# Performance work log

Hardware: AMD Instinct MI355X
Metric: run time of the kernel (lower is better)

Reference implementation:

```python
import jax, jax.numpy as jnp
import numpy as np

# Coefficient form of the 16 differentiable binary logic ops:
# op(a,b) = c0 + c1*a + c2*b + c3*a*b  (algebraically identical to bin_op_s's stacked einsum)
_COEF_NP = np.array([
    [0, 0, 0, 0],    # 0: zeros
    [0, 0, 0, 1],    # 1: a*b
    [0, 1, 0, -1],   # 2: a*(1-b)
    [0, 1, 0, 0],    # 3: a
    [0, 0, 1, -1],   # 4: (1-a)*b
    [0, 0, 1, 0],    # 5: b
    [0, 1, 1, -2],   # 6: xor
    [0, 1, 1, -1],   # 7: or
    [1, -1, -1, 1],  # 8: nor
    [1, -1, -1, 2],  # 9: xnor
    [1, 0, -1, 0],   # 10: 1-b
    [1, 0, -1, 1],   # 11: b=>a
    [1, -1, 0, 0],   # 12: 1-a
    [1, -1, 0, 1],   # 13: a=>b
    [1, 0, 0, -1],   # 14: nand
    [1, 0, 0, 0],    # 15: ones
], dtype=np.float32)
COEF = jnp.asarray(_COEF_NP)

TREE_DEPTH = 3
NUM_CLASSES = 10
TAU = 10.0
K = 32
BATCH = 128


def _conv_tree(x, leaf_idx, w):
    # x: [B,C,H,W]; leaf_idx: [O,8] int32 into C*9 unfolded patch dim; w: [O,7,16]
    B, C, H, W = x.shape
    xp = jnp.pad(x, ((0, 0), (0, 0), (1, 1), (1, 1)))
    # unfold (kernel=3, stride=1, pad=1): torch ordering is c*9 + spatial
    pats = jnp.stack([xp[:, :, di:di + H, dj:dj + W]
                      for di in range(3) for dj in range(3)], axis=2)  # [B,C,9,H,W]
    pats = pats.reshape(B, C * 9, H * W).transpose(0, 2, 1)            # [B,L,C*9]
    cur = pats[:, :, leaf_idx]                                         # [B,L,O,8]
    sw = jax.nn.softmax(w, axis=-1)                                    # training-mode soft gates
    coef = jnp.einsum('ogk,kc->ogc', sw, COEF)                         # [O,7,4]
    for level in range(TREE_DEPTH):
        a = cur[..., 0::2]
        b = cur[..., 1::2]                                             # [B,L,O,n]
        n = a.shape[-1]
        off = 2 ** level - 1                                           # faithful to original gate indexing
        c = coef[:, off:off + n]                                       # [O,n,4]
        cur = c[..., 0] + c[..., 1] * a + c[..., 2] * b + c[..., 3] * (a * b)
    out = cur[..., 0]                                                  # [B,L,O]
    return out.transpose(0, 2, 1).reshape(B, -1, H, W)


def _orpool(x):
    B, C, H, W = x.shape
    return x.reshape(B, C, H // 2, 2, W // 2, 2).max(axis=(3, 5))


def _difflogic(x, ca, cb, w):
    # x: [B,D]; ca/cb: [O]; w: [O,16]
    a = x[:, ca]
    b = x[:, cb]
    c = jax.nn.softmax(w, axis=-1) @ COEF                              # [O,4]
    return c[:, 0] + c[:, 1] * a + c[:, 2] * b + c[:, 3] * (a * b)


def _forward(x, w1, w2, w3, w4, fw1, fw2, fw3,
             l1, l2, l3, l4, ca1, cb1, ca2, cb2, ca3, cb3):
    # threshold-encode to 9 binary channels (bilinear resize to 32x32 is identity here)
    xb = jnp.concatenate([(x > (i + 1) / 4).astype(jnp.float32) for i in range(3)], axis=1)
    h = xb
    for li, w in ((l1, w1), (l2, w2), (l3, w3), (l4, w4)):
        h = _orpool(_conv_tree(h, li, w))
    h = h.reshape(h.shape[0], -1)                                      # [B, 4096]
    h = _difflogic(h, ca1, cb1, fw1)
    h = _difflogic(h, ca2, cb2, fw2)
    h = _difflogic(h, ca3, cb3, fw3)
    return h.reshape(h.shape[0], NUM_CLASSES, -1).sum(-1) / TAU


def _make_leaf_idx(in_ch, out_ch, rng):
    idx = np.zeros((out_ch, 8), np.int32)
    for c in range(out_ch):
        chans = rng.permutation(in_ch)[:2]
        parts = [ch * 9 + rng.permutation(9)[:4] for ch in chans]
        idx[c] = np.concatenate(parts)
    return jnp.asarray(idx)


def _unique_connections(in_dim, out_dim, rng):
    x = np.arange(in_dim, dtype=np.int64)
    a, b = x[::2], x[1::2]
    m = min(len(a), len(b)); a, b = a[:m], b[:m]
    if len(a) < out_dim:
        a = np.concatenate([a, x[1::2]]); b = np.concatenate([b, x[2::2]])
        m = min(len(a), len(b)); a, b = a[:m], b[:m]
    offset = 2
    while out_dim > len(a) > offset:
        a = np.concatenate([a, x[:-offset]]); b = np.concatenate([b, x[offset:]])
        offset += 1
    a, b = a[:out_dim], b[:out_dim]
    perm = rng.permutation(out_dim)
    return jnp.asarray(a[perm]), jnp.asarray(b[perm])


def setup_inputs() -> dict:
    key = jax.random.key(0)
    rng = np.random.default_rng(0)
    ks = jax.random.split(key, 8)
    x = jax.random.uniform(ks[0], (BATCH, 3, 32, 32), dtype=jnp.float32)
    chans = [(9, K), (K, 4 * K), (4 * K, 16 * K), (16 * K, 32 * K)]
    w1, w2, w3, w4 = [jax.random.normal(ks[1 + i], (oc, 7, 16), dtype=jnp.float32)
                      for i, (_, oc) in enumerate(chans)]
    l1, l2, l3, l4 = [_make_leaf_idx(ic, oc, rng) for ic, oc in chans]
    fc_in = 32 * K * 4
    fdims = [(fc_in, 1280 * K), (1280 * K, 640 * K), (640 * K, 320 * K)]
    fw1, fw2, fw3 = [jax.random.normal(ks[5 + i], (od, 16), dtype=jnp.float32)
                     for i, (_, od) in enumerate(fdims)]
    (ca1, cb1), (ca2, cb2), (ca3, cb3) = [_unique_connections(i, o, rng) for i, o in fdims]
    return dict(x=x, w1=w1, w2=w2, w3=w3, w4=w4, fw1=fw1, fw2=fw2, fw3=fw3,
                l1=l1, l2=l2, l3=l3, l4=l4,
                ca1=ca1, cb1=cb1, ca2=ca2, cb2=cb2, ca3=ca3, cb3=cb3)


def reference(x, w1, w2, w3, w4, fw1, fw2, fw3,
              l1, l2, l3, l4, ca1, cb1, ca2, cb2, ca3, cb3):
    return _forward(x, w1, w2, w3, w4, fw1, fw2, fw3,
                    l1, l2, l3, l4, ca1, cb1, ca2, cb2, ca3, cb3)
```

## Files before the change

kernel.cpp:

```cpp
#include <hip/hip_runtime.h>
#include <math.h>


typedef _Float16 h2 __attribute__((ext_vector_type(2)));

__constant__ float c_coef_tbl[16][4] = {
    {0, 0, 0, 0}, {0, 0, 0, 1}, {0, 1, 0, -1}, {0, 1, 0, 0},
    {0, 0, 1, -1}, {0, 0, 1, 0}, {0, 1, 1, -2}, {0, 1, 1, -1},
    {1, -1, -1, 1}, {1, -1, -1, 2}, {1, 0, -1, 0}, {1, 0, -1, 1},
    {1, -1, 0, 0}, {1, -1, 0, 1}, {1, 0, 0, -1}, {1, 0, 0, 0}};

__device__ __forceinline__ float4 softmax_coef(const float* __restrict__ wr) {
  float m = -1e30f;
#pragma unroll
  for (int k = 0; k < 16; ++k) m = fmaxf(m, wr[k]);
  float e[16], s = 0.f;
#pragma unroll
  for (int k = 0; k < 16; ++k) { e[k] = __expf(wr[k] - m); s += e[k]; }
  float inv = 1.f / s;
  float c0 = 0.f, c1 = 0.f, c2 = 0.f, c3 = 0.f;
#pragma unroll
  for (int k = 0; k < 16; ++k) {
    c0 += e[k] * c_coef_tbl[k][0];
    c1 += e[k] * c_coef_tbl[k][1];
    c2 += e[k] * c_coef_tbl[k][2];
    c3 += e[k] * c_coef_tbl[k][3];
  }
  return make_float4(c0 * inv, c1 * inv, c2 * inv, c3 * inv);
}

__device__ __forceinline__ float gate_eval(float4 c, float a, float b) {
  return c.x + c.y * a + c.z * b + c.w * (a * b);
}

__global__ void prep_all(const float* __restrict__ w1, const float* __restrict__ w2,
                         const float* __restrict__ w3, const float* __restrict__ w4,
                         const float* __restrict__ fw1, const float* __restrict__ fw2,
                         const float* __restrict__ fw3,
                         const int* __restrict__ ca1, const int* __restrict__ cb1,
                         const int* __restrict__ ca2, const int* __restrict__ cb2,
                         const int* __restrict__ ca3, const int* __restrict__ cb3,
                         float4* __restrict__ coefC,
                         unsigned short* __restrict__ midx16,
                         _Float16* __restrict__ mcoefh) {
  int g = blockIdx.x * blockDim.x + threadIdx.x;
  if (g < 71680) {
    int o = g / 7;
    int s = g - o * 7;
    float4 c;
    if (s < 4) {
      int k = (s < 2) ? ca3[o] : cb3[o];
      int j = (s & 1) ? cb2[k] : ca2[k];
      midx16[o * 8 + s * 2]     = (unsigned short)ca1[j];
      midx16[o * 8 + s * 2 + 1] = (unsigned short)cb1[j];
      c = softmax_coef(fw1 + j * 16);
    } else if (s < 6) {
      int k = (s == 4) ? ca3[o] : cb3[o];
      c = softmax_coef(fw2 + k * 16);
    } else {
      c = softmax_coef(fw3 + o * 16);
    }
    _Float16* mc = mcoefh + o * 28 + s * 4;
    mc[0] = (_Float16)c.x; mc[1] = (_Float16)c.y;
    mc[2] = (_Float16)c.z; mc[3] = (_Float16)c.w;
  } else if (g < 78464) {
    int gg = g - 71680;
    int base = gg;
    const float* w;
    if (gg < 128)       {               w = w1; }
    else if (gg < 640)  { gg -= 128;    w = w2; }
    else if (gg < 2688) { gg -= 640;    w = w3; }
    else                { gg -= 2688;   w = w4; }
    coefC[base] = softmax_coef(w + ((gg >> 2) * 7 + (gg & 3)) * 16);
  }
}

__device__ __forceinline__ h2 gateh(const h2* c, h2 a, h2 b) {
  return c[0] + c[1] * a + c[2] * b + c[3] * (a * b);
}

__device__ __forceinline__ float4 dec_cf(uint2 u) {
  h2 p0, p1;
  *(unsigned*)&p0 = u.x;
  *(unsigned*)&p1 = u.y;
  return make_float4((float)p0[0], (float)p0[1], (float)p1[0], (float)p1[1]);
}

template <int C, int H, int W, int OC, bool DUP>
__device__ void stage(const h2* __restrict__ in, h2* __restrict__ outD,
                      _Float16* __restrict__ outP,
                      const int* __restrict__ leaf,
                      const float4* __restrict__ coef, int tid) {
  constexpr int Hp = H + 2, Wp = W + 2;
  constexpr int PH = H / 2, PW = W / 2;
  constexpr int NPOS = PH * PW;
  constexpr int TPO = 1024 / OC;
  constexpr int ITER = NPOS / TPO;
  constexpr int OWp = PW + 2;
  constexpr int OHWp = (PH + 2) * (PW + 2);

  int oc = tid / TPO;
  int lane = tid % TPO;

  int toff[8];
#pragma unroll
  for (int l = 0; l < 8; ++l) {
    int k = leaf[oc * 8 + l];
    int cc = k / 9;
    int p = k - 9 * cc;
    int di = p / 3;
    int dj = p - 3 * di;
    toff[l] = cc * (Hp * Wp) + di * Wp + dj;
  }
  h2 ch[4][4];
#pragma unroll
  for (int r = 0; r < 4; ++r) {
    float4 c = coef[oc * 4 + r];
    _Float16 x0 = (_Float16)c.x, x1 = (_Float16)c.y,
             x2 = (_Float16)c.z, x3 = (_Float16)c.w;
    ch[r][0][0] = x0; ch[r][0][1] = x0;
    ch[r][1][0] = x1; ch[r][1][1] = x1;
    ch[r][2][0] = x2; ch[r][2][1] = x2;
    ch[r][3][0] = x3; ch[r][3][1] = x3;
  }

#pragma unroll
  for (int it = 0; it < ITER; ++it) {
    int pos = lane + it * TPO;
    int pw = pos % PW, ph = pos / PW;
    h2 o01[2];
#pragma unroll
    for (int py = 0; py < 2; ++py) {
      int pbase = (2 * ph + py) * Wp + 2 * pw;
      h2 lv[8];
#pragma unroll
      for (int l = 0; l < 8; ++l) lv[l] = in[toff[l] + pbase];
      h2 t0 = gateh(ch[0], lv[0], lv[1]);
      h2 t1 = gateh(ch[1], lv[2], lv[3]);
      h2 t2 = gateh(ch[2], lv[4], lv[5]);
      h2 t3 = gateh(ch[3], lv[6], lv[7]);
      h2 u0 = gateh(ch[1], t0, t1);
      h2 u1 = gateh(ch[2], t2, t3);
      o01[py] = gateh(ch[3], u0, u1);
    }
    _Float16 m0 = o01[0][0] > o01[1][0] ? o01[0][0] : o01[1][0];
    _Float16 m1 = o01[0][1] > o01[1][1] ? o01[0][1] : o01[1][1];
    _Float16 v = m0 > m1 ? m0 : m1;
    if (DUP) {
      _Float16* oh = (_Float16*)outD;
      int cell = oc * OHWp + (ph + 1) * OWp + (pw + 1);
      oh[2 * cell] = v;
      oh[2 * cell - 1] = v;
    } else {
      outP[oc * NPOS + ph * PW + pw] = v;
    }
  }
}

__device__ __forceinline__ void zero_h2(h2* p, int n, int tid) {
  for (int i = tid; i < n; i += 1024) p[i] = h2{(_Float16)0, (_Float16)0};
}

__global__ __launch_bounds__(1024) void mega(
    const float* __restrict__ x, const float4* __restrict__ coefC,
    const int* __restrict__ l1, const int* __restrict__ l2,
    const int* __restrict__ l3, const int* __restrict__ l4,
    const unsigned short* __restrict__ midx16,
    const _Float16* __restrict__ mcoefh, float* __restrict__ out) {
  __shared__ h2 A[12800];
  __shared__ h2 B[18432];
  __shared__ float red[16][10];
  int tid = threadIdx.x;
  int b = blockIdx.x;

  zero_h2(A, 10404, tid);
  zero_h2(B, 10368, tid);
  __syncthreads();
  const float* xb_ = x + b * 3072;
  for (int cell = tid; cell < 9 * 34 * 34; cell += 1024) {
    int j = cell % 34;
    int t = cell / 34;
    int i = t % 34;
    int c9 = t / 34;
    int th = c9 / 3, c = c9 - 3 * th;
    float thr = (float)(th + 1) * 0.25f;
    _Float16 lo = (_Float16)0, hi = (_Float16)0;
    if (i >= 1 && i <= 32) {
      const float* row = xb_ + c * 1024 + (i - 1) * 32;
      if (j >= 1 && j <= 32) lo = (_Float16)((row[j - 1] > thr) ? 1.f : 0.f);
      if (j <= 31)           hi = (_Float16)((row[j] > thr) ? 1.f : 0.f);
    }
    A[cell] = h2{lo, hi};
  }
  __syncthreads();

  stage<9, 32, 32, 32, true>(A, B, nullptr, l1, coefC, tid);
  __syncthreads();
  zero_h2(A, 12800, tid);
  __syncthreads();
  stage<32, 16, 16, 128, true>(B, A, nullptr, l2, coefC + 128, tid);
  __syncthreads();
  zero_h2(B, 18432, tid);
  __syncthreads();
  stage<128, 8, 8, 512, true>(A, B, nullptr, l3, coefC + 640, tid);
  __syncthreads();
  _Float16* Ah = (_Float16*)A;
  stage<512, 4, 4, 1024, false>(B, nullptr, Ah, l4, coefC + 2688, tid);
  __syncthreads();

  const uint4* mi = (const uint4*)midx16;
  const uint2* mc = (const uint2*)mcoefh;
  int wid = tid >> 6;
#pragma unroll
  for (int k = 0; k < 10; ++k) {
    int o = k * 1024 + tid;
    uint4 I = mi[o];
    const uint2* cfp = mc + o * 7;
    float L0 = gate_eval(dec_cf(cfp[0]), (float)Ah[I.x & 0xffff], (float)Ah[I.x >> 16]);
    float L1 = gate_eval(dec_cf(cfp[1]), (float)Ah[I.y & 0xffff], (float)Ah[I.y >> 16]);
    float L2 = gate_eval(dec_cf(cfp[2]), (float)Ah[I.z & 0xffff], (float)Ah[I.z >> 16]);
    float L3 = gate_eval(dec_cf(cfp[3]), (float)Ah[I.w & 0xffff], (float)Ah[I.w >> 16]);
    float M0 = gate_eval(dec_cf(cfp[4]), L0, L1);
    float M1 = gate_eval(dec_cf(cfp[5]), L2, L3);
    float y = gate_eval(dec_cf(cfp[6]), M0, M1);
#pragma unroll
    for (int m = 32; m > 0; m >>= 1) y += __shfl_xor(y, m, 64);
    if ((tid & 63) == 0) red[wid][k] = y;
  }
  __syncthreads();
  if (tid < 10) {
    float s = 0.f;
#pragma unroll
    for (int w = 0; w < 16; ++w) s += red[w][tid];
    out[b * 10 + tid] = s * 0.1f;
  }
}

extern "C" void kernel_launch(void* const* d_in, const int* in_sizes, int n_in,
                              void* d_out, int out_size, void* d_ws, size_t ws_size,
                              hipStream_t stream) {
  const float* x   = (const float*)d_in[0];
  const float* w1  = (const float*)d_in[1];
  const float* w2  = (const float*)d_in[2];
  const float* w3  = (const float*)d_in[3];
  const float* w4  = (const float*)d_in[4];
  const float* fw1 = (const float*)d_in[5];
  const float* fw2 = (const float*)d_in[6];
  const float* fw3 = (const float*)d_in[7];
  const int* l1  = (const int*)d_in[8];
  const int* l2  = (const int*)d_in[9];
  const int* l3  = (const int*)d_in[10];
  const int* l4  = (const int*)d_in[11];
  const int* ca1 = (const int*)d_in[12];
  const int* cb1 = (const int*)d_in[13];
  const int* ca2 = (const int*)d_in[14];
  const int* cb2 = (const int*)d_in[15];
  const int* ca3 = (const int*)d_in[16];
  const int* cb3 = (const int*)d_in[17];

  char* ws = (char*)d_ws;
  float4*         coefC  = (float4*)ws;
  unsigned short* midx16 = (unsigned short*)(ws + 108544);
  _Float16*       mcoefh = (_Float16*)(ws + 108544 + 163840);

  prep_all<<<307, 256, 0, stream>>>(w1, w2, w3, w4, fw1, fw2, fw3,
                                    ca1, cb1, ca2, cb2, ca3, cb3,
                                    coefC, midx16, mcoefh);
  mega<<<128, 1024, 0, stream>>>(x, coefC, l1, l2, l3, l4, midx16, mcoefh,
                                 (float*)d_out);
}
```

Measured before the change: 62.84 us.

## Split each sample across two cooperative blocks with global-memory stages and pair flags

Replaces the one-block-per-sample LDS megakernel with a cooperative launch of 256 blocks, where two blocks share each sample and each computes half the output channels of every conv stage. Intermediate activations move from shared memory to global workspace, and a pairwise flag barrier synchronises the partner blocks between stages. The conv stages also switch from packed half2 math on padded layouts to scalar fp32 gate evaluation with explicit bounds checks, and binarisation is fused into stage 1. This is meant to use all CUs, but it adds global-memory traffic, spin-wait synchronisation and recomputation of leaf offsets per job.

```diff
diff --git a/kernel.cpp b/kernel.cpp
--- a/kernel.cpp
+++ b/kernel.cpp
@@ -2,7 +2,10 @@
 #include <math.h>
 
 
-typedef _Float16 h2 __attribute__((ext_vector_type(2)));
+typedef _Float16 h16;
+typedef _Float16 h2v __attribute__((ext_vector_type(2)));
+
+#define NTHR 1024
 
 __constant__ float c_coef_tbl[16][4] = {
     {0, 0, 0, 0}, {0, 0, 0, 1}, {0, 1, 0, -1}, {0, 1, 0, 0},
@@ -31,6 +34,12 @@
 
 __device__ __forceinline__ float gate_eval(float4 c, float a, float b) {
   return c.x + c.y * a + c.z * b + c.w * (a * b);
+}
+__device__ __forceinline__ float4 dec_cf(uint2 u) {
+  h2v p0, p1;
+  *(unsigned*)&p0 = u.x;
+  *(unsigned*)&p1 = u.y;
+  return make_float4((float)p0[0], (float)p0[1], (float)p1[0], (float)p1[1]);
 }
 
 __global__ void prep_all(const float* __restrict__ w1, const float* __restrict__ w2,
@@ -42,8 +51,10 @@
                          const int* __restrict__ ca3, const int* __restrict__ cb3,
                          float4* __restrict__ coefC,
                          unsigned short* __restrict__ midx16,
-                         _Float16* __restrict__ mcoefh) {
+                         _Float16* __restrict__ mcoefh,
+                         unsigned int* __restrict__ flags) {
   int g = blockIdx.x * blockDim.x + threadIdx.x;
+  if (g < 256) flags[g] = 0u;
   if (g < 71680) {
     int o = g / 7;
     int s = g - o * 7;
@@ -67,172 +78,150 @@
     int gg = g - 71680;
     int base = gg;
     const float* w;
-    if (gg < 128)       {               w = w1; }
-    else if (gg < 640)  { gg -= 128;    w = w2; }
-    else if (gg < 2688) { gg -= 640;    w = w3; }
-    else                { gg -= 2688;   w = w4; }
+    if (gg < 128)       {             w = w1; }
+    else if (gg < 640)  { gg -= 128;  w = w2; }
+    else if (gg < 2688) { gg -= 640;  w = w3; }
+    else                { gg -= 2688; w = w4; }
     coefC[base] = softmax_coef(w + ((gg >> 2) * 7 + (gg & 3)) * 16);
   }
 }
 
-__device__ __forceinline__ h2 gateh(const h2* c, h2 a, h2 b) {
-  return c[0] + c[1] * a + c[2] * b + c[3] * (a * b);
-}
-
-__device__ __forceinline__ float4 dec_cf(uint2 u) {
-  h2 p0, p1;
-  *(unsigned*)&p0 = u.x;
-  *(unsigned*)&p1 = u.y;
-  return make_float4((float)p0[0], (float)p0[1], (float)p1[0], (float)p1[1]);
-}
-
-template <int C, int H, int W, int OC, bool DUP>
-__device__ void stage(const h2* __restrict__ in, h2* __restrict__ outD,
-                      _Float16* __restrict__ outP,
-                      const int* __restrict__ leaf,
-                      const float4* __restrict__ coef, int tid) {
-  constexpr int Hp = H + 2, Wp = W + 2;
-  constexpr int PH = H / 2, PW = W / 2;
+__device__ __forceinline__ void psync(unsigned int* flags, int me, int pa,
+                                      unsigned int s, int tid) {
+  __syncthreads();
+  if (tid == 0) {
+    __threadfence();
+    __hip_atomic_store(&flags[me], s, __ATOMIC_RELEASE, __HIP_MEMORY_SCOPE_AGENT);
+    while (__hip_atomic_load(&flags[pa], __ATOMIC_ACQUIRE,
+                             __HIP_MEMORY_SCOPE_AGENT) < s) {
+      __builtin_amdgcn_s_sleep(2);
+    }
+  }
+  __syncthreads();
+}
+
+template <int C, int H, int W, int OC, bool BIN>
+__device__ void stage(const h16* __restrict__ in, const float* __restrict__ xsrc,
+                      h16* __restrict__ outp, const int* __restrict__ leaf,
+                      const float4* __restrict__ coef, int role, int tid) {
+  constexpr int PH = H / 2, PW = W / 2, HW = H * W;
   constexpr int NPOS = PH * PW;
-  constexpr int TPO = 1024 / OC;
-  constexpr int ITER = NPOS / TPO;
-  constexpr int OWp = PW + 2;
-  constexpr int OHWp = (PH + 2) * (PW + 2);
-
-  int oc = tid / TPO;
-  int lane = tid % TPO;
-
-  int toff[8];
-#pragma unroll
-  for (int l = 0; l < 8; ++l) {
-    int k = leaf[oc * 8 + l];
-    int cc = k / 9;
-    int p = k - 9 * cc;
-    int di = p / 3;
-    int dj = p - 3 * di;
-    toff[l] = cc * (Hp * Wp) + di * Wp + dj;
-  }
-  h2 ch[4][4];
-#pragma unroll
-  for (int r = 0; r < 4; ++r) {
-    float4 c = coef[oc * 4 + r];
-    _Float16 x0 = (_Float16)c.x, x1 = (_Float16)c.y,
-             x2 = (_Float16)c.z, x3 = (_Float16)c.w;
-    ch[r][0][0] = x0; ch[r][0][1] = x0;
-    ch[r][1][0] = x1; ch[r][1][1] = x1;
-    ch[r][2][0] = x2; ch[r][2][1] = x2;
-    ch[r][3][0] = x3; ch[r][3][1] = x3;
-  }
-
-#pragma unroll
+  constexpr int NJ = (OC / 2) * NPOS;
+  constexpr int ITER = NJ / NTHR;
+  int ocBase = role * (OC / 2);
+#pragma unroll 2
   for (int it = 0; it < ITER; ++it) {
-    int pos = lane + it * TPO;
+    int job = it * NTHR + tid;
+    int pos = job % NPOS;
+    int oc = ocBase + job / NPOS;
     int pw = pos % PW, ph = pos / PW;
-    h2 o01[2];
+
+    int cc[8], di[8], dj[8];
+#pragma unroll
+    for (int l = 0; l < 8; ++l) {
+      int k = leaf[oc * 8 + l];
+      cc[l] = k / 9;
+      int p = k - 9 * cc[l];
+      di[l] = p / 3;
+      dj[l] = p - 3 * di[l];
+    }
+    float4 c0 = coef[oc * 4 + 0];
+    float4 c1 = coef[oc * 4 + 1];
+    float4 c2 = coef[oc * 4 + 2];
+    float4 c3 = coef[oc * 4 + 3];
+
+    float best = -1e30f;
 #pragma unroll
     for (int py = 0; py < 2; ++py) {
-      int pbase = (2 * ph + py) * Wp + 2 * pw;
-      h2 lv[8];
-#pragma unroll
-      for (int l = 0; l < 8; ++l) lv[l] = in[toff[l] + pbase];
-      h2 t0 = gateh(ch[0], lv[0], lv[1]);
-      h2 t1 = gateh(ch[1], lv[2], lv[3]);
-      h2 t2 = gateh(ch[2], lv[4], lv[5]);
-      h2 t3 = gateh(ch[3], lv[6], lv[7]);
-      h2 u0 = gateh(ch[1], t0, t1);
-      h2 u1 = gateh(ch[2], t2, t3);
-      o01[py] = gateh(ch[3], u0, u1);
-    }
-    _Float16 m0 = o01[0][0] > o01[1][0] ? o01[0][0] : o01[1][0];
-    _Float16 m1 = o01[0][1] > o01[1][1] ? o01[0][1] : o01[1][1];
-    _Float16 v = m0 > m1 ? m0 : m1;
-    if (DUP) {
-      _Float16* oh = (_Float16*)outD;
-      int cell = oc * OHWp + (ph + 1) * OWp + (pw + 1);
-      oh[2 * cell] = v;
-      oh[2 * cell - 1] = v;
-    } else {
-      outP[oc * NPOS + ph * PW + pw] = v;
-    }
-  }
-}
-
-__device__ __forceinline__ void zero_h2(h2* p, int n, int tid) {
-  for (int i = tid; i < n; i += 1024) p[i] = h2{(_Float16)0, (_Float16)0};
-}
-
-__global__ __launch_bounds__(1024) void mega(
+#pragma unroll
+      for (int px = 0; px < 2; ++px) {
+        int i = 2 * ph + py, j = 2 * pw + px;
+        float lv[8];
+#pragma unroll
+        for (int l = 0; l < 8; ++l) {
+          int ii = i + di[l] - 1, jj = j + dj[l] - 1;
+          float v = 0.f;
+          if ((unsigned)ii < (unsigned)H && (unsigned)jj < (unsigned)W) {
+            if (BIN) {
+              int bc = cc[l] % 3;
+              float thr = (float)(cc[l] / 3 + 1) * 0.25f;
+              v = (xsrc[bc * 1024 + ii * 32 + jj] > thr) ? 1.f : 0.f;
+            } else {
+              v = (float)in[cc[l] * HW + ii * W + jj];
+            }
+          }
+          lv[l] = v;
+        }
+        float t0 = gate_eval(c0, lv[0], lv[1]);
+        float t1 = gate_eval(c1, lv[2], lv[3]);
+        float t2 = gate_eval(c2, lv[4], lv[5]);
+        float t3 = gate_eval(c3, lv[6], lv[7]);
+        float u0 = gate_eval(c1, t0, t1);
+        float u1 = gate_eval(c2, t2, t3);
+        best = fmaxf(best, gate_eval(c3, u0, u1));
+      }
+    }
+    outp[oc * NPOS + pos] = (h16)best;
+  }
+}
+
+__global__ __launch_bounds__(1024) void coop(
     const float* __restrict__ x, const float4* __restrict__ coefC,
     const int* __restrict__ l1, const int* __restrict__ l2,
     const int* __restrict__ l3, const int* __restrict__ l4,
     const unsigned short* __restrict__ midx16,
-    const _Float16* __restrict__ mcoefh, float* __restrict__ out) {
-  __shared__ h2 A[12800];
-  __shared__ h2 B[18432];
-  __shared__ float red[16][10];
+    const _Float16* __restrict__ mcoefh,
+    h16* __restrict__ s1, h16* __restrict__ s2,
+    h16* __restrict__ s3, h16* __restrict__ s4,
+    unsigned int* __restrict__ flags, float* __restrict__ out) {
+  __shared__ float red[16];
   int tid = threadIdx.x;
-  int b = blockIdx.x;
-
-  zero_h2(A, 10404, tid);
-  zero_h2(B, 10368, tid);
-  __syncthreads();
-  const float* xb_ = x + b * 3072;
-  for (int cell = tid; cell < 9 * 34 * 34; cell += 1024) {
-    int j = cell % 34;
-    int t = cell / 34;
-    int i = t % 34;
-    int c9 = t / 34;
-    int th = c9 / 3, c = c9 - 3 * th;
-    float thr = (float)(th + 1) * 0.25f;
-    _Float16 lo = (_Float16)0, hi = (_Float16)0;
-    if (i >= 1 && i <= 32) {
-      const float* row = xb_ + c * 1024 + (i - 1) * 32;
-      if (j >= 1 && j <= 32) lo = (_Float16)((row[j - 1] > thr) ? 1.f : 0.f);
-      if (j <= 31)           hi = (_Float16)((row[j] > thr) ? 1.f : 0.f);
-    }
-    A[cell] = h2{lo, hi};
-  }
-  __syncthreads();
-
-  stage<9, 32, 32, 32, true>(A, B, nullptr, l1, coefC, tid);
-  __syncthreads();
-  zero_h2(A, 12800, tid);
-  __syncthreads();
-  stage<32, 16, 16, 128, true>(B, A, nullptr, l2, coefC + 128, tid);
-  __syncthreads();
-  zero_h2(B, 18432, tid);
-  __syncthreads();
-  stage<128, 8, 8, 512, true>(A, B, nullptr, l3, coefC + 640, tid);
-  __syncthreads();
-  _Float16* Ah = (_Float16*)A;
-  stage<512, 4, 4, 1024, false>(B, nullptr, Ah, l4, coefC + 2688, tid);
-  __syncthreads();
+  int me = blockIdx.x;
+  int g = me & 127;
+  int role = me >> 7;
+  int pa = me ^ 128;
+
+  const float* xg = x + g * 3072;
+  h16* b1 = s1 + g * 8192;
+  h16* b2 = s2 + g * 8192;
+  h16* b3 = s3 + g * 8192;
+  h16* b4 = s4 + g * 4096;
+
+  stage<9, 32, 32, 32, true>(nullptr, xg, b1, l1, coefC, role, tid);
+  psync(flags, me, pa, 1, tid);
+  stage<32, 16, 16, 128, false>(b1, nullptr, b2, l2, coefC + 128, role, tid);
+  psync(flags, me, pa, 2, tid);
+  stage<128, 8, 8, 512, false>(b2, nullptr, b3, l3, coefC + 640, role, tid);
+  psync(flags, me, pa, 3, tid);
+  stage<512, 4, 4, 1024, false>(b3, nullptr, b4, l4, coefC + 2688, role, tid);
+  psync(flags, me, pa, 4, tid);
 
   const uint4* mi = (const uint4*)midx16;
   const uint2* mc = (const uint2*)mcoefh;
-  int wid = tid >> 6;
-#pragma unroll
-  for (int k = 0; k < 10; ++k) {
-    int o = k * 1024 + tid;
+#pragma unroll
+  for (int k = 0; k < 5; ++k) {
+    int cls = role * 5 + k;
+    int o = cls * 1024 + tid;
     uint4 I = mi[o];
     const uint2* cfp = mc + o * 7;
-    float L0 = gate_eval(dec_cf(cfp[0]), (float)Ah[I.x & 0xffff], (float)Ah[I.x >> 16]);
-    float L1 = gate_eval(dec_cf(cfp[1]), (float)Ah[I.y & 0xffff], (float)Ah[I.y >> 16]);
-    float L2 = gate_eval(dec_cf(cfp[2]), (float)Ah[I.z & 0xffff], (float)Ah[I.z >> 16]);
-    float L3 = gate_eval(dec_cf(cfp[3]), (float)Ah[I.w & 0xffff], (float)Ah[I.w >> 16]);
+    float L0 = gate_eval(dec_cf(cfp[0]), (float)b4[I.x & 0xffff], (float)b4[I.x >> 16]);
+    float L1 = gate_eval(dec_cf(cfp[1]), (float)b4[I.y & 0xffff], (float)b4[I.y >> 16]);
+    float L2 = gate_eval(dec_cf(cfp[2]), (float)b4[I.z & 0xffff], (float)b4[I.z >> 16]);
+    float L3 = gate_eval(dec_cf(cfp[3]), (float)b4[I.w & 0xffff], (float)b4[I.w >> 16]);
     float M0 = gate_eval(dec_cf(cfp[4]), L0, L1);
     float M1 = gate_eval(dec_cf(cfp[5]), L2, L3);
     float y = gate_eval(dec_cf(cfp[6]), M0, M1);
 #pragma unroll
     for (int m = 32; m > 0; m >>= 1) y += __shfl_xor(y, m, 64);
-    if ((tid & 63) == 0) red[wid][k] = y;
-  }
-  __syncthreads();
-  if (tid < 10) {
-    float s = 0.f;
-#pragma unroll
-    for (int w = 0; w < 16; ++w) s += red[w][tid];
-    out[b * 10 + tid] = s * 0.1f;
+    if ((tid & 63) == 0) red[tid >> 6] = y;
+    __syncthreads();
+    if (tid == 0) {
+      float s = 0.f;
+#pragma unroll
+      for (int w = 0; w < 16; ++w) s += red[w];
+      out[g * 10 + cls] = s * 0.1f;
+    }
+    __syncthreads();
   }
 }
 
@@ -257,15 +246,23 @@
   const int* cb2 = (const int*)d_in[15];
   const int* ca3 = (const int*)d_in[16];
   const int* cb3 = (const int*)d_in[17];
+  float* out = (float*)d_out;
 
   char* ws = (char*)d_ws;
   float4*         coefC  = (float4*)ws;
   unsigned short* midx16 = (unsigned short*)(ws + 108544);
-  _Float16*       mcoefh = (_Float16*)(ws + 108544 + 163840);
+  _Float16*       mcoefh = (_Float16*)(ws + 272384);
+  unsigned int*   flags  = (unsigned int*)(ws + 845824);
+  h16*            s1b    = (h16*)(ws + 846848);
+  h16*            s2b    = (h16*)(ws + 846848 + 2097152);
+  h16*            s3b    = (h16*)(ws + 846848 + 2 * 2097152);
+  h16*            s4b    = (h16*)(ws + 846848 + 3 * 2097152);
 
   prep_all<<<307, 256, 0, stream>>>(w1, w2, w3, w4, fw1, fw2, fw3,
                                     ca1, cb1, ca2, cb2, ca3, cb3,
-                                    coefC, midx16, mcoefh);
-  mega<<<128, 1024, 0, stream>>>(x, coefC, l1, l2, l3, l4, midx16, mcoefh,
-                                 (float*)d_out);
-}
+                                    coefC, midx16, mcoefh, flags);
+
+  void* args[] = {&x, &coefC, &l1, &l2, &l3, &l4, &midx16, &mcoefh,
+                  &s1b, &s2b, &s3b, &s4b, &flags, &out};
+  hipLaunchCooperativeKernel((void*)coop, dim3(256), dim3(1024), args, 0, stream);
+}
```

Result: slower. 161.3 us (+156.7%).

## Split each sample across two cooperative blocks with global-memory staging and pair flags

Applied to the files above, without the earlier changes.

Each batch sample was handled by one 1024-thread block using shared-memory ping-pong buffers. Now two blocks per sample each take half the output channels and half the classes of every stage, doubling the grid to 256 blocks so more CUs are used. Intermediates move from LDS to global workspace, and the paired blocks synchronize through release/acquire flags in a cooperative launch. This trades higher latency on the gather-heavy stage reads, plus the cross-block spin barriers, for twice the parallelism.

```diff
diff --git a/kernel.cpp b/kernel.cpp
--- a/kernel.cpp
+++ b/kernel.cpp
@@ -2,6 +2,7 @@
 #include <math.h>
 
 
+typedef _Float16 h16;
 typedef _Float16 h2 __attribute__((ext_vector_type(2)));
 
 __constant__ float c_coef_tbl[16][4] = {
@@ -31,6 +32,15 @@
 
 __device__ __forceinline__ float gate_eval(float4 c, float a, float b) {
   return c.x + c.y * a + c.z * b + c.w * (a * b);
+}
+__device__ __forceinline__ float4 dec_cf(uint2 u) {
+  h2 p0, p1;
+  *(unsigned*)&p0 = u.x;
+  *(unsigned*)&p1 = u.y;
+  return make_float4((float)p0[0], (float)p0[1], (float)p1[0], (float)p1[1]);
+}
+__device__ __forceinline__ h2 gateh(const h2* c, h2 a, h2 b) {
+  return c[0] + c[1] * a + c[2] * b + c[3] * (a * b);
 }
 
 __global__ void prep_all(const float* __restrict__ w1, const float* __restrict__ w2,
@@ -42,8 +52,10 @@
                          const int* __restrict__ ca3, const int* __restrict__ cb3,
                          float4* __restrict__ coefC,
                          unsigned short* __restrict__ midx16,
-                         _Float16* __restrict__ mcoefh) {
+                         _Float16* __restrict__ mcoefh,
+                         unsigned int* __restrict__ flags) {
   int g = blockIdx.x * blockDim.x + threadIdx.x;
+  if (g < 256) flags[g] = 0u;
   if (g < 71680) {
     int o = g / 7;
     int s = g - o * 7;
@@ -67,39 +79,42 @@
     int gg = g - 71680;
     int base = gg;
     const float* w;
-    if (gg < 128)       {               w = w1; }
-    else if (gg < 640)  { gg -= 128;    w = w2; }
-    else if (gg < 2688) { gg -= 640;    w = w3; }
-    else                { gg -= 2688;   w = w4; }
+    if (gg < 128)       {             w = w1; }
+    else if (gg < 640)  { gg -= 128;  w = w2; }
+    else if (gg < 2688) { gg -= 640;  w = w3; }
+    else                { gg -= 2688; w = w4; }
     coefC[base] = softmax_coef(w + ((gg >> 2) * 7 + (gg & 3)) * 16);
   }
 }
 
-__device__ __forceinline__ h2 gateh(const h2* c, h2 a, h2 b) {
-  return c[0] + c[1] * a + c[2] * b + c[3] * (a * b);
-}
-
-__device__ __forceinline__ float4 dec_cf(uint2 u) {
-  h2 p0, p1;
-  *(unsigned*)&p0 = u.x;
-  *(unsigned*)&p1 = u.y;
-  return make_float4((float)p0[0], (float)p0[1], (float)p1[0], (float)p1[1]);
+__device__ __forceinline__ void psync(unsigned int* flags, int me, int pa,
+                                      unsigned int s, int tid) {
+  __syncthreads();
+  if (tid == 0) {
+    __threadfence();
+    __hip_atomic_store(&flags[me], s, __ATOMIC_RELEASE, __HIP_MEMORY_SCOPE_AGENT);
+    while (__hip_atomic_load(&flags[pa], __ATOMIC_ACQUIRE,
+                             __HIP_MEMORY_SCOPE_AGENT) < s) {
+      __builtin_amdgcn_s_sleep(2);
+    }
+  }
+  __syncthreads();
 }
 
 template <int C, int H, int W, int OC, bool DUP>
 __device__ void stage(const h2* __restrict__ in, h2* __restrict__ outD,
-                      _Float16* __restrict__ outP,
+                      h16* __restrict__ outP,
                       const int* __restrict__ leaf,
-                      const float4* __restrict__ coef, int tid) {
+                      const float4* __restrict__ coef, int role, int tid) {
   constexpr int Hp = H + 2, Wp = W + 2;
   constexpr int PH = H / 2, PW = W / 2;
   constexpr int NPOS = PH * PW;
-  constexpr int TPO = 1024 / OC;
+  constexpr int TPO = 2048 / OC;
   constexpr int ITER = NPOS / TPO;
   constexpr int OWp = PW + 2;
   constexpr int OHWp = (PH + 2) * (PW + 2);
 
-  int oc = tid / TPO;
+  int oc = role * (OC / 2) + tid / TPO;
   int lane = tid % TPO;
 
   int toff[8];
@@ -147,7 +162,7 @@
     _Float16 m1 = o01[0][1] > o01[1][1] ? o01[0][1] : o01[1][1];
     _Float16 v = m0 > m1 ? m0 : m1;
     if (DUP) {
-      _Float16* oh = (_Float16*)outD;
+      h16* oh = (h16*)outD;
       int cell = oc * OHWp + (ph + 1) * OWp + (pw + 1);
       oh[2 * cell] = v;
       oh[2 * cell - 1] = v;
@@ -157,27 +172,39 @@
   }
 }
 
-__device__ __forceinline__ void zero_h2(h2* p, int n, int tid) {
-  for (int i = tid; i < n; i += 1024) p[i] = h2{(_Float16)0, (_Float16)0};
-}
-
-__global__ __launch_bounds__(1024) void mega(
+__global__ __launch_bounds__(1024) void coop(
     const float* __restrict__ x, const float4* __restrict__ coefC,
     const int* __restrict__ l1, const int* __restrict__ l2,
     const int* __restrict__ l3, const int* __restrict__ l4,
     const unsigned short* __restrict__ midx16,
-    const _Float16* __restrict__ mcoefh, float* __restrict__ out) {
-  __shared__ h2 A[12800];
-  __shared__ h2 B[18432];
-  __shared__ float red[16][10];
+    const _Float16* __restrict__ mcoefh,
+    h2* __restrict__ xbB, h2* __restrict__ s1B, h2* __restrict__ s2B,
+    h2* __restrict__ s3B, h16* __restrict__ s4B,
+    unsigned int* __restrict__ flags, float* __restrict__ out) {
+  __shared__ float red[16];
   int tid = threadIdx.x;
-  int b = blockIdx.x;
-
-  zero_h2(A, 10404, tid);
-  zero_h2(B, 10368, tid);
-  __syncthreads();
-  const float* xb_ = x + b * 3072;
-  for (int cell = tid; cell < 9 * 34 * 34; cell += 1024) {
+  int me = blockIdx.x;
+  int g = me & 127;
+  int role = me >> 7;
+  int pa = me ^ 128;
+
+  const float* xg = x + g * 3072;
+  h2*  xb = xbB + g * 10404;
+  h2*  b1 = s1B + g * 10368;
+  h2*  b2 = s2B + g * 12800;
+  h2*  b3 = s3B + g * 18432;
+  h16* b4 = s4B + g * 4096;
+
+  {
+    float4* z1 = (float4*)b1;
+    float4* z2 = (float4*)b2;
+    float4* z3 = (float4*)b3;
+    float4 zz = make_float4(0.f, 0.f, 0.f, 0.f);
+    for (int i = role * 1296 + tid; i < (role + 1) * 1296; i += 1024) z1[i] = zz;
+    for (int i = role * 1600 + tid; i < (role + 1) * 1600; i += 1024) z2[i] = zz;
+    for (int i = role * 2304 + tid; i < (role + 1) * 2304; i += 1024) z3[i] = zz;
+  }
+  for (int cell = role * 5202 + tid; cell < role * 5202 + 5202; cell += 1024) {
     int j = cell % 34;
     int t = cell / 34;
     int i = t % 34;
@@ -186,53 +213,49 @@
     float thr = (float)(th + 1) * 0.25f;
     _Float16 lo = (_Float16)0, hi = (_Float16)0;
     if (i >= 1 && i <= 32) {
-      const float* row = xb_ + c * 1024 + (i - 1) * 32;
+      const float* row = xg + c * 1024 + (i - 1) * 32;
       if (j >= 1 && j <= 32) lo = (_Float16)((row[j - 1] > thr) ? 1.f : 0.f);
       if (j <= 31)           hi = (_Float16)((row[j] > thr) ? 1.f : 0.f);
     }
-    A[cell] = h2{lo, hi};
-  }
-  __syncthreads();
-
-  stage<9, 32, 32, 32, true>(A, B, nullptr, l1, coefC, tid);
-  __syncthreads();
-  zero_h2(A, 12800, tid);
-  __syncthreads();
-  stage<32, 16, 16, 128, true>(B, A, nullptr, l2, coefC + 128, tid);
-  __syncthreads();
-  zero_h2(B, 18432, tid);
-  __syncthreads();
-  stage<128, 8, 8, 512, true>(A, B, nullptr, l3, coefC + 640, tid);
-  __syncthreads();
-  _Float16* Ah = (_Float16*)A;
-  stage<512, 4, 4, 1024, false>(B, nullptr, Ah, l4, coefC + 2688, tid);
-  __syncthreads();
+    xb[cell] = h2{lo, hi};
+  }
+  psync(flags, me, pa, 1, tid);
+
+  stage<9, 32, 32, 32, true>(xb, b1, nullptr, l1, coefC, role, tid);
+  psync(flags, me, pa, 2, tid);
+  stage<32, 16, 16, 128, true>(b1, b2, nullptr, l2, coefC + 128, role, tid);
+  psync(flags, me, pa, 3, tid);
+  stage<128, 8, 8, 512, true>(b2, b3, nullptr, l3, coefC + 640, role, tid);
+  psync(flags, me, pa, 4, tid);
+  stage<512, 4, 4, 1024, false>(b3, nullptr, b4, l4, coefC + 2688, role, tid);
+  psync(flags, me, pa, 5, tid);
 
   const uint4* mi = (const uint4*)midx16;
   const uint2* mc = (const uint2*)mcoefh;
-  int wid = tid >> 6;
-#pragma unroll
-  for (int k = 0; k < 10; ++k) {
-    int o = k * 1024 + tid;
+#pragma unroll
+  for (int k = 0; k < 5; ++k) {
+    int cls = role * 5 + k;
+    int o = cls * 1024 + tid;
     uint4 I = mi[o];
     const uint2* cfp = mc + o * 7;
-    float L0 = gate_eval(dec_cf(cfp[0]), (float)Ah[I.x & 0xffff], (float)Ah[I.x >> 16]);
-    float L1 = gate_eval(dec_cf(cfp[1]), (float)Ah[I.y & 0xffff], (float)Ah[I.y >> 16]);
-    float L2 = gate_eval(dec_cf(cfp[2]), (float)Ah[I.z & 0xffff], (float)Ah[I.z >> 16]);
-    float L3 = gate_eval(dec_cf(cfp[3]), (float)Ah[I.w & 0xffff], (float)Ah[I.w >> 16]);
+    float L0 = gate_eval(dec_cf(cfp[0]), (float)b4[I.x & 0xffff], (float)b4[I.x >> 16]);
+    float L1 = gate_eval(dec_cf(cfp[1]), (float)b4[I.y & 0xffff], (float)b4[I.y >> 16]);
+    float L2 = gate_eval(dec_cf(cfp[2]), (float)b4[I.z & 0xffff], (float)b4[I.z >> 16]);
+    float L3 = gate_eval(dec_cf(cfp[3]), (float)b4[I.w & 0xffff], (float)b4[I.w >> 16]);
     float M0 = gate_eval(dec_cf(cfp[4]), L0, L1);
     float M1 = gate_eval(dec_cf(cfp[5]), L2, L3);
     float y = gate_eval(dec_cf(cfp[6]), M0, M1);
 #pragma unroll
     for (int m = 32; m > 0; m >>= 1) y += __shfl_xor(y, m, 64);
-    if ((tid & 63) == 0) red[wid][k] = y;
-  }
-  __syncthreads();
-  if (tid < 10) {
-    float s = 0.f;
-#pragma unroll
-    for (int w = 0; w < 16; ++w) s += red[w][tid];
-    out[b * 10 + tid] = s * 0.1f;
+    if ((tid & 63) == 0) red[tid >> 6] = y;
+    __syncthreads();
+    if (tid == 0) {
+      float s = 0.f;
+#pragma unroll
+      for (int w = 0; w < 16; ++w) s += red[w];
+      out[g * 10 + cls] = s * 0.1f;
+    }
+    __syncthreads();
   }
 }
 
@@ -257,15 +280,24 @@
   const int* cb2 = (const int*)d_in[15];
   const int* ca3 = (const int*)d_in[16];
   const int* cb3 = (const int*)d_in[17];
+  float* out = (float*)d_out;
 
   char* ws = (char*)d_ws;
   float4*         coefC  = (float4*)ws;
   unsigned short* midx16 = (unsigned short*)(ws + 108544);
-  _Float16*       mcoefh = (_Float16*)(ws + 108544 + 163840);
+  _Float16*       mcoefh = (_Float16*)(ws + 272384);
+  unsigned int*   flags  = (unsigned int*)(ws + 845824);
+  h2*  xbB = (h2*)(ws + 846848);
+  h2*  s1B = (h2*)(ws + 6173696);
+  h2*  s2B = (h2*)(ws + 11482112);
+  h2*  s3B = (h2*)(ws + 18035712);
+  h16* s4B = (h16*)(ws + 27472896);
 
   prep_all<<<307, 256, 0, stream>>>(w1, w2, w3, w4, fw1, fw2, fw3,
                                     ca1, cb1, ca2, cb2, ca3, cb3,
-                                    coefC, midx16, mcoefh);
-  mega<<<128, 1024, 0, stream>>>(x, coefC, l1, l2, l3, l4, midx16, mcoefh,
-                                 (float*)d_out);
-}
+                                    coefC, midx16, mcoefh, flags);
+
+  void* args[] = {&x, &coefC, &l1, &l2, &l3, &l4, &midx16, &mcoefh,
+                  &xbB, &s1B, &s2B, &s3B, &s4B, &flags, &out};
+  hipLaunchCooperativeKernel((void*)coop, dim3(256), dim3(1024), args, 0, stream);
+}
```

After: 163.9 us. 161% more time.

## Give each conv stage its own padded shared buffer and compute stage 4 in fp32

Applied to the files above, without the earlier changes.

Replaces the two ping-pong shared buffers with a dedicated shared array per stage. Each array uses a padded per-channel stride (an odd number of h2 words), which is meant to reduce LDS bank conflicts. The buffers are zeroed once up front, which removes the re-zeroing passes and two barriers between stages. Stage 3 now writes a compact unpadded fp16 output, and stage 4 is a custom one-thread-per-channel loop in fp32 with explicit bounds checks. The cost is more total LDS, some branchy scalar loads in stage 4, and fp32 instead of packed fp16 arithmetic for that stage.

```diff
diff --git a/kernel.cpp b/kernel.cpp
--- a/kernel.cpp
+++ b/kernel.cpp
@@ -2,6 +2,7 @@
 #include <math.h>
 
 
+typedef _Float16 h16;
 typedef _Float16 h2 __attribute__((ext_vector_type(2)));
 
 __constant__ float c_coef_tbl[16][4] = {
@@ -31,6 +32,15 @@
 
 __device__ __forceinline__ float gate_eval(float4 c, float a, float b) {
   return c.x + c.y * a + c.z * b + c.w * (a * b);
+}
+__device__ __forceinline__ float4 dec_cf(uint2 u) {
+  h2 p0, p1;
+  *(unsigned*)&p0 = u.x;
+  *(unsigned*)&p1 = u.y;
+  return make_float4((float)p0[0], (float)p0[1], (float)p1[0], (float)p1[1]);
+}
+__device__ __forceinline__ h2 gateh(const h2* c, h2 a, h2 b) {
+  return c[0] + c[1] * a + c[2] * b + c[3] * (a * b);
 }
 
 __global__ void prep_all(const float* __restrict__ w1, const float* __restrict__ w2,
@@ -67,37 +77,25 @@
     int gg = g - 71680;
     int base = gg;
     const float* w;
-    if (gg < 128)       {               w = w1; }
-    else if (gg < 640)  { gg -= 128;    w = w2; }
-    else if (gg < 2688) { gg -= 640;    w = w3; }
-    else                { gg -= 2688;   w = w4; }
+    if (gg < 128)       {             w = w1; }
+    else if (gg < 640)  { gg -= 128;  w = w2; }
+    else if (gg < 2688) { gg -= 640;  w = w3; }
+    else                { gg -= 2688; w = w4; }
     coefC[base] = softmax_coef(w + ((gg >> 2) * 7 + (gg & 3)) * 16);
   }
 }
 
-__device__ __forceinline__ h2 gateh(const h2* c, h2 a, h2 b) {
-  return c[0] + c[1] * a + c[2] * b + c[3] * (a * b);
-}
-
-__device__ __forceinline__ float4 dec_cf(uint2 u) {
-  h2 p0, p1;
-  *(unsigned*)&p0 = u.x;
-  *(unsigned*)&p1 = u.y;
-  return make_float4((float)p0[0], (float)p0[1], (float)p1[0], (float)p1[1]);
-}
-
-template <int C, int H, int W, int OC, bool DUP>
+template <int C, int H, int W, int OC, int IPS, int OPS, bool OUTDUP>
 __device__ void stage(const h2* __restrict__ in, h2* __restrict__ outD,
-                      _Float16* __restrict__ outP,
+                      h16* __restrict__ outP,
                       const int* __restrict__ leaf,
                       const float4* __restrict__ coef, int tid) {
-  constexpr int Hp = H + 2, Wp = W + 2;
+  constexpr int Wp = W + 2;
   constexpr int PH = H / 2, PW = W / 2;
   constexpr int NPOS = PH * PW;
   constexpr int TPO = 1024 / OC;
   constexpr int ITER = NPOS / TPO;
   constexpr int OWp = PW + 2;
-  constexpr int OHWp = (PH + 2) * (PW + 2);
 
   int oc = tid / TPO;
   int lane = tid % TPO;
@@ -110,7 +108,7 @@
     int p = k - 9 * cc;
     int di = p / 3;
     int dj = p - 3 * di;
-    toff[l] = cc * (Hp * Wp) + di * Wp + dj;
+    toff[l] = cc * IPS + di * Wp + dj;
   }
   h2 ch[4][4];
 #pragma unroll
@@ -146,19 +144,15 @@
     _Float16 m0 = o01[0][0] > o01[1][0] ? o01[0][0] : o01[1][0];
     _Float16 m1 = o01[0][1] > o01[1][1] ? o01[0][1] : o01[1][1];
     _Float16 v = m0 > m1 ? m0 : m1;
-    if (DUP) {
-      _Float16* oh = (_Float16*)outD;
-      int cell = oc * OHWp + (ph + 1) * OWp + (pw + 1);
+    if (OUTDUP) {
+      h16* oh = (h16*)outD;
+      int cell = oc * OPS + (ph + 1) * OWp + (pw + 1);
       oh[2 * cell] = v;
       oh[2 * cell - 1] = v;
     } else {
       outP[oc * NPOS + ph * PW + pw] = v;
     }
   }
-}
-
-__device__ __forceinline__ void zero_h2(h2* p, int n, int tid) {
-  for (int i = tid; i < n; i += 1024) p[i] = h2{(_Float16)0, (_Float16)0};
 }
 
 __global__ __launch_bounds__(1024) void mega(
@@ -167,45 +161,92 @@
     const int* __restrict__ l3, const int* __restrict__ l4,
     const unsigned short* __restrict__ midx16,
     const _Float16* __restrict__ mcoefh, float* __restrict__ out) {
-  __shared__ h2 A[12800];
-  __shared__ h2 B[18432];
+  __shared__ __align__(16) h2 XB[9 * 1157];
+  __shared__ __align__(16) h2 S1[32 * 325];
+  __shared__ __align__(16) h2 S2[128 * 101];
+  __shared__ __align__(16) h16 S3[512 * 16];
+  __shared__ __align__(16) h16 S4[1024 * 4];
   __shared__ float red[16][10];
   int tid = threadIdx.x;
   int b = blockIdx.x;
 
-  zero_h2(A, 10404, tid);
-  zero_h2(B, 10368, tid);
-  __syncthreads();
-  const float* xb_ = x + b * 3072;
-  for (int cell = tid; cell < 9 * 34 * 34; cell += 1024) {
-    int j = cell % 34;
-    int t = cell / 34;
-    int i = t % 34;
-    int c9 = t / 34;
+  {
+    float4* z1 = (float4*)S1;
+    float4* z2 = (float4*)S2;
+    float4 zz = make_float4(0.f, 0.f, 0.f, 0.f);
+    for (int i = tid; i < 2600; i += 1024) z1[i] = zz;
+    for (int i = tid; i < 3232; i += 1024) z2[i] = zz;
+  }
+  const float* xg = x + b * 3072;
+  for (int cell = tid; cell < 9 * 1157; cell += 1024) {
+    int c9 = cell / 1157;
+    int rem = cell - c9 * 1157;
+    if (rem >= 1156) continue;
+    int i = rem / 34, j = rem - 34 * (rem / 34);
     int th = c9 / 3, c = c9 - 3 * th;
     float thr = (float)(th + 1) * 0.25f;
     _Float16 lo = (_Float16)0, hi = (_Float16)0;
     if (i >= 1 && i <= 32) {
-      const float* row = xb_ + c * 1024 + (i - 1) * 32;
+      const float* row = xg + c * 1024 + (i - 1) * 32;
       if (j >= 1 && j <= 32) lo = (_Float16)((row[j - 1] > thr) ? 1.f : 0.f);
       if (j <= 31)           hi = (_Float16)((row[j] > thr) ? 1.f : 0.f);
     }
-    A[cell] = h2{lo, hi};
-  }
-  __syncthreads();
-
-  stage<9, 32, 32, 32, true>(A, B, nullptr, l1, coefC, tid);
-  __syncthreads();
-  zero_h2(A, 12800, tid);
-  __syncthreads();
-  stage<32, 16, 16, 128, true>(B, A, nullptr, l2, coefC + 128, tid);
-  __syncthreads();
-  zero_h2(B, 18432, tid);
-  __syncthreads();
-  stage<128, 8, 8, 512, true>(A, B, nullptr, l3, coefC + 640, tid);
-  __syncthreads();
-  _Float16* Ah = (_Float16*)A;
-  stage<512, 4, 4, 1024, false>(B, nullptr, Ah, l4, coefC + 2688, tid);
+    XB[cell] = h2{lo, hi};
+  }
+  __syncthreads();
+
+  stage<9, 32, 32, 32, 1157, 325, true>(XB, S1, nullptr, l1, coefC, tid);
+  __syncthreads();
+  stage<32, 16, 16, 128, 325, 101, true>(S1, S2, nullptr, l2, coefC + 128, tid);
+  __syncthreads();
+  stage<128, 8, 8, 512, 101, 0, false>(S2, nullptr, S3, l3, coefC + 640, tid);
+  __syncthreads();
+
+  {
+    int oc = tid;
+    int cc[8], di[8], dj[8];
+#pragma unroll
+    for (int l = 0; l < 8; ++l) {
+      int k = l4[oc * 8 + l];
+      cc[l] = k / 9;
+      int p = k - 9 * cc[l];
+      di[l] = p / 3;
+      dj[l] = p - 3 * di[l];
+    }
+    float4 c0 = coefC[2688 + oc * 4 + 0];
+    float4 c1 = coefC[2688 + oc * 4 + 1];
+    float4 c2 = coefC[2688 + oc * 4 + 2];
+    float4 c3 = coefC[2688 + oc * 4 + 3];
+#pragma unroll
+    for (int pos = 0; pos < 4; ++pos) {
+      int pw = pos & 1, ph = pos >> 1;
+      float best = -1e30f;
+#pragma unroll
+      for (int py = 0; py < 2; ++py) {
+#pragma unroll
+        for (int px = 0; px < 2; ++px) {
+          int i = 2 * ph + py, j = 2 * pw + px;
+          float lv[8];
+#pragma unroll
+          for (int l = 0; l < 8; ++l) {
+            int ii = i + di[l] - 1, jj = j + dj[l] - 1;
+            float v = 0.f;
+            if ((unsigned)ii < 4u && (unsigned)jj < 4u)
+              v = (float)S3[cc[l] * 16 + ii * 4 + jj];
+            lv[l] = v;
+          }
+          float t0 = gate_eval(c0, lv[0], lv[1]);
+          float t1 = gate_eval(c1, lv[2], lv[3]);
+          float t2 = gate_eval(c2, lv[4], lv[5]);
+          float t3 = gate_eval(c3, lv[6], lv[7]);
+          float u0 = gate_eval(c1, t0, t1);
+          float u1 = gate_eval(c2, t2, t3);
+          best = fmaxf(best, gate_eval(c3, u0, u1));
+        }
+      }
+      S4[oc * 4 + pos] = (h16)best;
+    }
+  }
   __syncthreads();
 
   const uint4* mi = (const uint4*)midx16;
@@ -216,10 +257,10 @@
     int o = k * 1024 + tid;
     uint4 I = mi[o];
     const uint2* cfp = mc + o * 7;
-    float L0 = gate_eval(dec_cf(cfp[0]), (float)Ah[I.x & 0xffff], (float)Ah[I.x >> 16]);
-    float L1 = gate_eval(dec_cf(cfp[1]), (float)Ah[I.y & 0xffff], (float)Ah[I.y >> 16]);
-    float L2 = gate_eval(dec_cf(cfp[2]), (float)Ah[I.z & 0xffff], (float)Ah[I.z >> 16]);
-    float L3 = gate_eval(dec_cf(cfp[3]), (float)Ah[I.w & 0xffff], (float)Ah[I.w >> 16]);
+    float L0 = gate_eval(dec_cf(cfp[0]), (float)S4[I.x & 0xffff], (float)S4[I.x >> 16]);
+    float L1 = gate_eval(dec_cf(cfp[1]), (float)S4[I.y & 0xffff], (float)S4[I.y >> 16]);
+    float L2 = gate_eval(dec_cf(cfp[2]), (float)S4[I.z & 0xffff], (float)S4[I.z >> 16]);
+    float L3 = gate_eval(dec_cf(cfp[3]), (float)S4[I.w & 0xffff], (float)S4[I.w >> 16]);
     float M0 = gate_eval(dec_cf(cfp[4]), L0, L1);
     float M1 = gate_eval(dec_cf(cfp[5]), L2, L3);
     float y = gate_eval(dec_cf(cfp[6]), M0, M1);
```

Result: no change. 63.14 us (+0.5%).
